# Performance work log

Hardware: AMD Instinct MI355X
Metric: run time of the kernel (lower is better)

The kernel has to match this reference:

```python
import jax, jax.numpy as jnp
import numpy as np

VOCAB = 32000
HID = 2048
MAXLEN = 128


def setup_inputs() -> dict:
    key = jax.random.key(0)
    ks = jax.random.split(key, 16)
    s = 0.02
    return {
        "input_seq": jax.random.randint(ks[0], (1, 1), 0, VOCAB),
        "hidden": jax.random.normal(ks[1], (1, 1, HID), jnp.float32),
        "encoder_outputs": jax.random.normal(ks[2], (MAXLEN, HID), jnp.float32),
        "emb": jax.random.normal(ks[3], (VOCAB, HID), jnp.float32) * s,
        "attn_W": jax.random.normal(ks[4], (MAXLEN, 2 * HID), jnp.float32) * s,
        "attn_b": jnp.zeros((MAXLEN,), jnp.float32),
        "comb_W": jax.random.normal(ks[5], (HID, 2 * HID), jnp.float32) * s,
        "comb_b": jnp.zeros((HID,), jnp.float32),
        "W_ih": jax.random.normal(ks[6], (HID, HID), jnp.float32) * s,
        "W_hh": jax.random.normal(ks[7], (HID, HID), jnp.float32) * s,
        "b_ih": jnp.zeros((HID,), jnp.float32),
        "b_hh": jnp.zeros((HID,), jnp.float32),
        "out_W": jax.random.normal(ks[8], (VOCAB, HID), jnp.float32) * s,
        "out_b": jnp.zeros((VOCAB,), jnp.float32),
    }


def _rnn_step(x, h, W_ih, W_hh, b_ih, b_hh):
    # Elman RNN cell (tanh): seq_len=1 so output == new hidden. Shapes [1,1,H].
    return jnp.tanh(x @ W_ih.T + b_ih + h @ W_hh.T + b_hh)


def reference(input_seq, hidden, encoder_outputs, emb, attn_W, attn_b,
              comb_W, comb_b, W_ih, W_hh, b_ih, b_hh, out_W, out_b):
    tok = input_seq[0]                       # [1]
    x = emb[tok].reshape(1, 1, -1)           # [1,1,H]
    hidden = _rnn_step(x, hidden, W_ih, W_hh, b_ih, b_hh)   # [1,1,H]
    # second embedding of the decoder token (dropout is identity at eval)
    embedded = emb[tok].reshape(1, 1, -1)    # [1,1,H]
    attn_in = jnp.concatenate([embedded[0], hidden[0]], axis=1)   # [1,2H]
    attn_weights = jax.nn.softmax(attn_in @ attn_W.T + attn_b, axis=1)  # [1,L]
    attn_applied = attn_weights @ encoder_outputs                 # [1,H]
    o = jnp.concatenate([embedded[0], attn_applied], axis=1) @ comb_W.T + comb_b
    o = jax.nn.relu(o)[None]                 # [1,1,H]
    out_h = _rnn_step(o, hidden, W_ih, W_hh, b_ih, b_hh)          # [1,1,H]
    logits = out_h[0] @ out_W.T + out_b      # [1,VOCAB]
    return jax.nn.log_softmax(logits, axis=1)
```

## Files before the change

### kernel.cpp

```cpp
#include <hip/hip_runtime.h>
#include <math.h>

#define HID 2048
#define KQ (HID / 4)
#define MAXLEN 128
#define VOCAB 32000

__device__ __forceinline__ float wave_sum(float v) {
    #pragma unroll
    for (int m = 1; m < 64; m <<= 1) v += __shfl_xor(v, m, 64);
    return v;
}

__device__ __forceinline__ float dot4(float4 a, float4 b) {
    return a.x * b.x + a.y * b.y + a.z * b.z + a.w * b.w;
}

__device__ __forceinline__ float block_sum256(float v) {
    __shared__ float s[4];
    v = wave_sum(v);
    const int lane = threadIdx.x & 63, w = threadIdx.x >> 6;
    if (lane == 0) s[w] = v;
    __syncthreads();
    return s[0] + s[1] + s[2] + s[3];
}

__global__ __launch_bounds__(256)
void rnn_cell_kernel(const float* __restrict__ W1, const float* __restrict__ x1,
                     const int* __restrict__ tok,
                     const float* __restrict__ W2, const float* __restrict__ x2,
                     const float* __restrict__ b1, const float* __restrict__ b2,
                     float* __restrict__ out) {
    const int r = blockIdx.x, t = threadIdx.x;
    const float4* xa = (const float4*)(tok ? x1 + (size_t)tok[0] * HID : x1);
    const float4* xb = (const float4*)x2;
    const float4* w1 = (const float4*)(W1 + (size_t)r * HID);
    const float4* w2 = (const float4*)(W2 + (size_t)r * HID);
    float p = dot4(w1[t], xa[t]) + dot4(w1[t + 256], xa[t + 256])
            + dot4(w2[t], xb[t]) + dot4(w2[t + 256], xb[t + 256]);
    p = block_sum256(p);
    if (t == 0) out[r] = tanhf(p + b1[r] + b2[r]);
}

template<int ACT>
__global__ __launch_bounds__(256)
void concat_mv_kernel(const float* __restrict__ W,
                      const float* __restrict__ emb, const int* __restrict__ tok,
                      const float* __restrict__ xb, const float* __restrict__ b,
                      float* __restrict__ out) {
    const int r = blockIdx.x, t = threadIdx.x;
    const float4* xa = (const float4*)(emb + (size_t)tok[0] * HID);
    const float4* xv = (const float4*)xb;
    const float4* w  = (const float4*)(W + (size_t)r * 2 * HID);
    float p = dot4(w[t], xa[t]) + dot4(w[t + 256], xa[t + 256])
            + dot4(w[t + 512], xv[t]) + dot4(w[t + 768], xv[t + 256]);
    p = block_sum256(p);
    if (t == 0) {
        p += b[r];
        if (ACT == 2) p = fmaxf(p, 0.f);
        out[r] = p;
    }
}

__global__ __launch_bounds__(256)
void softmax_apply_kernel(const float* __restrict__ AL, const float* __restrict__ enc,
                          float* __restrict__ out) {
    __shared__ float sAL[MAXLEN];
    __shared__ float wts[MAXLEN];
    __shared__ float cs[4][64];
    const int t = threadIdx.x;
    if (t < MAXLEN) sAL[t] = AL[t];
    __syncthreads();
    float m = sAL[0];
    for (int l = 1; l < MAXLEN; ++l) m = fmaxf(m, sAL[l]);
    float s = 0.f;
    for (int l = 0; l < MAXLEN; ++l) s += expf(sAL[l] - m);
    if (t < MAXLEN) wts[t] = expf(sAL[t] - m) / s;
    __syncthreads();
    const int j  = blockIdx.x * 64 + (t & 63);
    const int l0 = t >> 6;
    float acc = 0.f;
    #pragma unroll 8
    for (int l = l0; l < MAXLEN; l += 4) acc += wts[l] * enc[(size_t)l * HID + j];
    cs[l0][t & 63] = acc;
    __syncthreads();
    if (t < 64) out[blockIdx.x * 64 + t] = cs[0][t] + cs[1][t] + cs[2][t] + cs[3][t];
}

__global__ __launch_bounds__(256)
void bigmv_kernel(const float* __restrict__ W, const float* __restrict__ x,
                  const float* __restrict__ b, float* __restrict__ out,
                  float* __restrict__ PE) {
    __shared__ float red[4];
    const int wid = threadIdx.x >> 6, lane = threadIdx.x & 63;
    const int r = blockIdx.x * 4 + wid;
    const float4* xv = (const float4*)x;
    const float4* w  = (const float4*)(W + (size_t)r * HID);
    float p = 0.f;
    #pragma unroll 8
    for (int i = lane; i < KQ; i += 64) p += dot4(w[i], xv[i]);
    p = wave_sum(p);
    if (lane == 0) {
        p += b[r];
        out[r] = p;
        red[wid] = expf(p);
    }
    __syncthreads();
    if (threadIdx.x == 0) PE[blockIdx.x] = red[0] + red[1] + red[2] + red[3];
}

__global__ __launch_bounds__(256)
void lse_apply_kernel(const float* __restrict__ PE, float* __restrict__ out) {
    const int t = threadIdx.x;
    float s = 0.f;
    for (int i = t; i < VOCAB / 4; i += 256) s += PE[i];
    const float lg = logf(block_sum256(s));
    out[blockIdx.x * 256 + t] -= lg;
}

extern "C" void kernel_launch(void* const* d_in, const int* in_sizes, int n_in,
                              void* d_out, int out_size, void* d_ws, size_t ws_size,
                              hipStream_t stream) {
    const int*   tok    = (const int*)  d_in[0];
    const float* hidden = (const float*)d_in[1];
    const float* enc    = (const float*)d_in[2];
    const float* emb    = (const float*)d_in[3];
    const float* attn_W = (const float*)d_in[4];
    const float* attn_b = (const float*)d_in[5];
    const float* comb_W = (const float*)d_in[6];
    const float* comb_b = (const float*)d_in[7];
    const float* W_ih   = (const float*)d_in[8];
    const float* W_hh   = (const float*)d_in[9];
    const float* b_ih   = (const float*)d_in[10];
    const float* b_hh   = (const float*)d_in[11];
    const float* out_W  = (const float*)d_in[12];
    const float* out_b  = (const float*)d_in[13];
    float* out = (float*)d_out;

    float* ws = (float*)d_ws;
    float* H1 = ws;
    float* AL = ws + 2048;
    float* AA = ws + 2176;
    float* O  = ws + 4224;
    float* OH = ws + 6272;
    float* PE = ws + 8320;

    rnn_cell_kernel<<<HID, 256, 0, stream>>>(W_ih, emb, tok, W_hh, hidden, b_ih, b_hh, H1);
    concat_mv_kernel<0><<<MAXLEN, 256, 0, stream>>>(attn_W, emb, tok, H1, attn_b, AL);
    softmax_apply_kernel<<<HID / 64, 256, 0, stream>>>(AL, enc, AA);
    concat_mv_kernel<2><<<HID, 256, 0, stream>>>(comb_W, emb, tok, AA, comb_b, O);
    rnn_cell_kernel<<<HID, 256, 0, stream>>>(W_ih, O, nullptr, W_hh, H1, b_ih, b_hh, OH);
    bigmv_kernel<<<VOCAB / 4, 256, 0, stream>>>(out_W, OH, out_b, out, PE);
    lse_apply_kernel<<<VOCAB / 256, 256, 0, stream>>>(PE, out);
}
```

Measured before the change: 89.20 us.

## Split concat matvecs to hoist embedding halves off the dependency chain

Each concatenated matvec (attention and combine) is split into an embedding half and a hidden/attention half. The embedding halves are computed early, fused into the first RNN kernel and into the attention-right kernel, so the dependent kernels on the critical path only read half as many weights. The vocab matvec also gets two independent accumulators for more memory-level parallelism. Kernel count stays at seven and extra workspace round-trips are added, so any gain depends on the shorter dependent-kernel chain.

```diff
diff --git a/kernel.cpp b/kernel.cpp
--- a/kernel.cpp
+++ b/kernel.cpp
@@ -25,46 +25,58 @@
     return s[0] + s[1] + s[2] + s[3];
 }
 
-__global__ __launch_bounds__(256)
-void rnn_cell_kernel(const float* __restrict__ W1, const float* __restrict__ x1,
-                     const int* __restrict__ tok,
-                     const float* __restrict__ W2, const float* __restrict__ x2,
-                     const float* __restrict__ b1, const float* __restrict__ b2,
-                     float* __restrict__ out) {
-    const int r = blockIdx.x, t = threadIdx.x;
-    const float4* xa = (const float4*)(tok ? x1 + (size_t)tok[0] * HID : x1);
-    const float4* xb = (const float4*)x2;
-    const float4* w1 = (const float4*)(W1 + (size_t)r * HID);
-    const float4* w2 = (const float4*)(W2 + (size_t)r * HID);
-    float p = dot4(w1[t], xa[t]) + dot4(w1[t + 256], xa[t + 256])
-            + dot4(w2[t], xb[t]) + dot4(w2[t + 256], xb[t + 256]);
-    p = block_sum256(p);
-    if (t == 0) out[r] = tanhf(p + b1[r] + b2[r]);
+__device__ __forceinline__ float row_dot2048(const float4* __restrict__ w,
+                                             const float4* __restrict__ x) {
+    const int t = threadIdx.x;
+    return dot4(w[t], x[t]) + dot4(w[t + 256], x[t + 256]);
 }
 
-template<int ACT>
 __global__ __launch_bounds__(256)
-void concat_mv_kernel(const float* __restrict__ W,
+void k1_rnn1_attnleft(const float* __restrict__ W_ih, const float* __restrict__ W_hh,
                       const float* __restrict__ emb, const int* __restrict__ tok,
-                      const float* __restrict__ xb, const float* __restrict__ b,
-                      float* __restrict__ out) {
-    const int r = blockIdx.x, t = threadIdx.x;
-    const float4* xa = (const float4*)(emb + (size_t)tok[0] * HID);
-    const float4* xv = (const float4*)xb;
-    const float4* w  = (const float4*)(W + (size_t)r * 2 * HID);
-    float p = dot4(w[t], xa[t]) + dot4(w[t + 256], xa[t + 256])
-            + dot4(w[t + 512], xv[t]) + dot4(w[t + 768], xv[t + 256]);
-    p = block_sum256(p);
-    if (t == 0) {
-        p += b[r];
-        if (ACT == 2) p = fmaxf(p, 0.f);
-        out[r] = p;
+                      const float* __restrict__ hidden,
+                      const float* __restrict__ b_ih, const float* __restrict__ b_hh,
+                      const float* __restrict__ attn_W, const float* __restrict__ attn_b,
+                      float* __restrict__ H1, float* __restrict__ ALe) {
+    const float4* xemb = (const float4*)(emb + (size_t)tok[0] * HID);
+    const int bid = blockIdx.x, t = threadIdx.x;
+    if (bid < HID) {
+        const float4* w1 = (const float4*)(W_ih + (size_t)bid * HID);
+        const float4* w2 = (const float4*)(W_hh + (size_t)bid * HID);
+        float p = row_dot2048(w1, xemb) + row_dot2048(w2, (const float4*)hidden);
+        p = block_sum256(p);
+        if (t == 0) H1[bid] = tanhf(p + b_ih[bid] + b_hh[bid]);
+    } else {
+        const int l = bid - HID;
+        const float4* w = (const float4*)(attn_W + (size_t)l * 2 * HID);
+        float p = block_sum256(row_dot2048(w, xemb));
+        if (t == 0) ALe[l] = p + attn_b[l];
     }
 }
 
 __global__ __launch_bounds__(256)
-void softmax_apply_kernel(const float* __restrict__ AL, const float* __restrict__ enc,
-                          float* __restrict__ out) {
+void k2_attnright_combleft(const float* __restrict__ attn_W,
+                           const float* __restrict__ comb_W, const float* __restrict__ comb_b,
+                           const float* __restrict__ emb, const int* __restrict__ tok,
+                           const float* __restrict__ H1, const float* __restrict__ ALe,
+                           float* __restrict__ AL, float* __restrict__ Oe) {
+    const int bid = blockIdx.x, t = threadIdx.x;
+    if (bid < MAXLEN) {
+        const float4* w = (const float4*)(attn_W + (size_t)bid * 2 * HID + HID);
+        float p = block_sum256(row_dot2048(w, (const float4*)H1));
+        if (t == 0) AL[bid] = ALe[bid] + p;
+    } else {
+        const int r = bid - MAXLEN;
+        const float4* xemb = (const float4*)(emb + (size_t)tok[0] * HID);
+        const float4* w = (const float4*)(comb_W + (size_t)r * 2 * HID);
+        float p = block_sum256(row_dot2048(w, xemb));
+        if (t == 0) Oe[r] = p + comb_b[r];
+    }
+}
+
+__global__ __launch_bounds__(256)
+void k3_softmax_apply(const float* __restrict__ AL, const float* __restrict__ enc,
+                      float* __restrict__ AA) {
     __shared__ float sAL[MAXLEN];
     __shared__ float wts[MAXLEN];
     __shared__ float cs[4][64];
@@ -84,22 +96,47 @@
     for (int l = l0; l < MAXLEN; l += 4) acc += wts[l] * enc[(size_t)l * HID + j];
     cs[l0][t & 63] = acc;
     __syncthreads();
-    if (t < 64) out[blockIdx.x * 64 + t] = cs[0][t] + cs[1][t] + cs[2][t] + cs[3][t];
+    if (t < 64) AA[blockIdx.x * 64 + t] = cs[0][t] + cs[1][t] + cs[2][t] + cs[3][t];
 }
 
 __global__ __launch_bounds__(256)
-void bigmv_kernel(const float* __restrict__ W, const float* __restrict__ x,
-                  const float* __restrict__ b, float* __restrict__ out,
-                  float* __restrict__ PE) {
+void k4_comb_right(const float* __restrict__ comb_W, const float* __restrict__ AA,
+                   const float* __restrict__ Oe, float* __restrict__ O) {
+    const int r = blockIdx.x, t = threadIdx.x;
+    const float4* w = (const float4*)(comb_W + (size_t)r * 2 * HID + HID);
+    float p = block_sum256(row_dot2048(w, (const float4*)AA));
+    if (t == 0) O[r] = fmaxf(Oe[r] + p, 0.f);
+}
+
+__global__ __launch_bounds__(256)
+void k5_rnn2(const float* __restrict__ W_ih, const float* __restrict__ W_hh,
+             const float* __restrict__ O, const float* __restrict__ H1,
+             const float* __restrict__ b_ih, const float* __restrict__ b_hh,
+             float* __restrict__ OH) {
+    const int r = blockIdx.x, t = threadIdx.x;
+    const float4* w1 = (const float4*)(W_ih + (size_t)r * HID);
+    const float4* w2 = (const float4*)(W_hh + (size_t)r * HID);
+    float p = row_dot2048(w1, (const float4*)O) + row_dot2048(w2, (const float4*)H1);
+    p = block_sum256(p);
+    if (t == 0) OH[r] = tanhf(p + b_ih[r] + b_hh[r]);
+}
+
+__global__ __launch_bounds__(256)
+void k6_bigmv(const float* __restrict__ W, const float* __restrict__ x,
+              const float* __restrict__ b, float* __restrict__ out,
+              float* __restrict__ PE) {
     __shared__ float red[4];
     const int wid = threadIdx.x >> 6, lane = threadIdx.x & 63;
     const int r = blockIdx.x * 4 + wid;
     const float4* xv = (const float4*)x;
     const float4* w  = (const float4*)(W + (size_t)r * HID);
-    float p = 0.f;
-    #pragma unroll 8
-    for (int i = lane; i < KQ; i += 64) p += dot4(w[i], xv[i]);
-    p = wave_sum(p);
+    float p0 = 0.f, p1 = 0.f;
+    #pragma unroll
+    for (int k = 0; k < 8; k += 2) {
+        p0 += dot4(w[lane + k * 64], xv[lane + k * 64]);
+        p1 += dot4(w[lane + (k + 1) * 64], xv[lane + (k + 1) * 64]);
+    }
+    float p = wave_sum(p0 + p1);
     if (lane == 0) {
         p += b[r];
         out[r] = p;
@@ -110,7 +147,7 @@
 }
 
 __global__ __launch_bounds__(256)
-void lse_apply_kernel(const float* __restrict__ PE, float* __restrict__ out) {
+void k7_lse_apply(const float* __restrict__ PE, float* __restrict__ out) {
     const int t = threadIdx.x;
     float s = 0.f;
     for (int i = t; i < VOCAB / 4; i += 256) s += PE[i];
@@ -137,19 +174,23 @@
     const float* out_b  = (const float*)d_in[13];
     float* out = (float*)d_out;
 
-    float* ws = (float*)d_ws;
-    float* H1 = ws;
-    float* AL = ws + 2048;
-    float* AA = ws + 2176;
-    float* O  = ws + 4224;
-    float* OH = ws + 6272;
-    float* PE = ws + 8320;
+    float* ws  = (float*)d_ws;
+    float* H1  = ws;
+    float* ALe = ws + 2048;
+    float* AL  = ws + 2176;
+    float* AA  = ws + 2304;
+    float* Oe  = ws + 4352;
+    float* O   = ws + 6400;
+    float* OH  = ws + 8448;
+    float* PE  = ws + 10496;
 
-    rnn_cell_kernel<<<HID, 256, 0, stream>>>(W_ih, emb, tok, W_hh, hidden, b_ih, b_hh, H1);
-    concat_mv_kernel<0><<<MAXLEN, 256, 0, stream>>>(attn_W, emb, tok, H1, attn_b, AL);
-    softmax_apply_kernel<<<HID / 64, 256, 0, stream>>>(AL, enc, AA);
-    concat_mv_kernel<2><<<HID, 256, 0, stream>>>(comb_W, emb, tok, AA, comb_b, O);
-    rnn_cell_kernel<<<HID, 256, 0, stream>>>(W_ih, O, nullptr, W_hh, H1, b_ih, b_hh, OH);
-    bigmv_kernel<<<VOCAB / 4, 256, 0, stream>>>(out_W, OH, out_b, out, PE);
-    lse_apply_kernel<<<VOCAB / 256, 256, 0, stream>>>(PE, out);
+    k1_rnn1_attnleft<<<HID + MAXLEN, 256, 0, stream>>>(W_ih, W_hh, emb, tok, hidden,
+                                                       b_ih, b_hh, attn_W, attn_b, H1, ALe);
+    k2_attnright_combleft<<<MAXLEN + HID, 256, 0, stream>>>(attn_W, comb_W, comb_b,
+                                                            emb, tok, H1, ALe, AL, Oe);
+    k3_softmax_apply<<<HID / 64, 256, 0, stream>>>(AL, enc, AA);
+    k4_comb_right<<<HID, 256, 0, stream>>>(comb_W, AA, Oe, O);
+    k5_rnn2<<<HID, 256, 0, stream>>>(W_ih, W_hh, O, H1, b_ih, b_hh, OH);
+    k6_bigmv<<<VOCAB / 4, 256, 0, stream>>>(out_W, OH, out_b, out, PE);
+    k7_lse_apply<<<VOCAB / 256, 256, 0, stream>>>(PE, out);
 }
```

After: 89.08 us. No clear change (-0.1%).
